# Kernel optimization log

Measured on AMD Instinct MI355X. Metric: run time of the kernel, lower is better.

The kernel has to match this reference:

```python
import jax, jax.numpy as jnp
import numpy as np

# db4 analysis filters (pywt convention); synthesis reuses same filters (orthogonal wavelet,
# correlation analysis + convolution synthesis gives perfect reconstruction under periodization).
DEC_LO = [-0.010597401784997278, 0.032883011666982945, 0.030841381835986965, -0.18703481171888114,
          -0.02798376941698385, 0.6308807679295904, 0.7148465705525415, 0.23037781330885523]
DEC_HI = [-0.23037781330885523, 0.7148465705525415, -0.6308807679295904, -0.02798376941698385,
          0.18703481171888114, 0.030841381835986965, -0.032883011666982945, -0.010597401784997278]
LEVELS = 3

def _analysis(x, filt):
    # a[n] = sum_k filt[k] * x[(2n+k) mod L]  (circular filter + downsample-by-2)
    y = sum(c * jnp.roll(x, -k, axis=-1) for k, c in enumerate(filt))
    return y[..., ::2]

def _synthesis(a, filt):
    # upsample-by-2 (zeros at odd positions) then circular convolution with filt
    u = jnp.zeros(a.shape[:-1] + (2 * a.shape[-1],), a.dtype).at[..., ::2].set(a)
    return sum(c * jnp.roll(u, k, axis=-1) for k, c in enumerate(filt))

def _decompose(z, levels):
    details, cur = [], z
    for _ in range(levels):
        details.append(_analysis(cur, DEC_HI))
        cur = _analysis(cur, DEC_LO)
    return cur, details

def _reconstruct(approx, details):
    cur = approx
    for d in reversed(details):
        cur = _synthesis(cur, DEC_LO) + _synthesis(d, DEC_HI)
    return cur

def _soft_threshold(c, lam_raw):
    # dynamic per-(batch,channel) threshold scaled by learnable softplus(lam_raw)
    lam = jax.nn.softplus(lam_raw) * jnp.mean(jnp.abs(c), axis=-1)  # [B,H]
    thr = jnp.sign(c) * jnp.maximum(jnp.abs(c) - lam[..., None], 0.0)
    return thr, lam

def _film(c, flow_raw, Wgb, bgb, Wg, bg):
    # FiLM gamma/beta from flow features, sigmoid-gated
    gb = flow_raw @ Wgb.T + bgb                      # [B, 2H]
    H = c.shape[1]
    gamma, beta = gb[:, :H], gb[:, H:]
    gate = jax.nn.sigmoid(flow_raw @ Wg + bg)[:, None, None]  # [B,1,1]
    return c * (1.0 + gate * gamma[:, :, None]) + gate * beta[:, :, None]

def setup_inputs() -> dict:
    key = jax.random.key(0)
    ks = jax.random.split(key, 8)
    B, L, C, Hd = 16, 4096, 64, 128
    x = jax.random.normal(ks[0], (B, L, C), jnp.float32)
    mask = jnp.ones((B, L), jnp.float32)
    flow_raw = jax.random.normal(ks[1], (B, 24), jnp.float32)
    W_in = jax.random.normal(ks[2], (Hd, C), jnp.float32) / np.sqrt(C)
    b_in = jnp.zeros((Hd,), jnp.float32)
    W_mix = jax.random.normal(ks[3], (Hd, Hd), jnp.float32) / np.sqrt(Hd)
    b_mix = jnp.zeros((Hd,), jnp.float32)
    lam_raw = jnp.full((LEVELS + 1,), 0.5413248538970947, jnp.float32)  # softplus^-1(1.0)
    film_Wgb = jax.random.normal(ks[4], (LEVELS + 1, 2 * Hd, 24), jnp.float32) * 0.05
    film_bgb = jnp.zeros((LEVELS + 1, 2 * Hd), jnp.float32)
    film_Wg = jax.random.normal(ks[5], (LEVELS + 1, 24), jnp.float32) * 0.05
    film_bg = jnp.zeros((LEVELS + 1,), jnp.float32)
    return dict(x=x, mask=mask, flow_raw=flow_raw, W_in=W_in, b_in=b_in, W_mix=W_mix, b_mix=b_mix,
                lam_raw=lam_raw, film_Wgb=film_Wgb, film_bgb=film_bgb, film_Wg=film_Wg, film_bg=film_bg)

def reference(x, mask, flow_raw, W_in, b_in, W_mix, b_mix, lam_raw, film_Wgb, film_bgb, film_Wg, film_bg):
    xp = x.transpose(0, 2, 1) * mask[:, None, :]               # [B,C,L]
    z = jnp.einsum('hc,bcl->bhl', W_in, xp) + b_in[:, None]    # input_proj (1x1 conv)
    approx, details = _decompose(z, LEVELS)
    approx = _film(approx, flow_raw, film_Wgb[0], film_bgb[0], film_Wg[0], film_bg[0])
    details = [_film(d, flow_raw, film_Wgb[i + 1], film_bgb[i + 1], film_Wg[i + 1], film_bg[i + 1])
               for i, d in enumerate(details)]
    approx_t, lam_a = _soft_threshold(approx, lam_raw[0])
    dts, lams = [], [lam_a]
    for i, d in enumerate(details):
        dt, lam_d = _soft_threshold(d, lam_raw[i + 1])
        dts.append(dt)
        lams.append(lam_d)
    z_rec = _reconstruct(approx_t, dts)
    mixed = jnp.einsum('gh,bhl->bgl', W_mix, z + z_rec) + b_mix[:, None]  # mix (1x1 conv)
    out = jax.nn.gelu(mixed, approximate=False)                 # torch nn.GELU is exact
    h_seq = out.transpose(0, 2, 1) * mask[..., None]            # [B,L,H]
    denom = jnp.clip(jnp.sum(mask, axis=1, keepdims=True), 1.0, None)
    h_pool = jnp.sum(h_seq * mask[..., None], axis=1) / denom   # masked mean pool [B,H]
    lam_cat = jnp.concatenate([l.reshape(l.shape[0], -1) for l in lams], axis=1)
    return h_seq, h_pool, jnp.mean(lam_cat, axis=1), jnp.max(lam_cat, axis=1)
```

## Files before the change

### kernel.cpp

```cpp
#include <hip/hip_runtime.h>
#include <math.h>

#define BB 16
#define LL 4096
#define CC 64
#define HD 128

typedef __attribute__((ext_vector_type(8))) short short8;
typedef __attribute__((ext_vector_type(8))) unsigned short ushort8;
typedef __attribute__((ext_vector_type(4))) float floatx4;

__constant__ float c_lo[8] = {
    -0.010597401784997278f, 0.032883011666982945f, 0.030841381835986965f,
    -0.18703481171888114f, -0.02798376941698385f, 0.6308807679295904f,
    0.7148465705525415f, 0.23037781330885523f};
__constant__ float c_hi[8] = {
    -0.23037781330885523f, 0.7148465705525415f, -0.6308807679295904f,
    -0.02798376941698385f, 0.18703481171888114f, 0.030841381835986965f,
    -0.032883011666982945f, -0.010597401784997278f};

__device__ __forceinline__ float gelu_exact(float x) {
    return 0.5f * x * (1.0f + erff(x * 0.70710678118654752440f));
}
__device__ __forceinline__ unsigned short f2b(float f) {
    unsigned int u = __float_as_uint(f);
    u = u + 0x7FFFu + ((u >> 16) & 1u);
    return (unsigned short)(u >> 16);
}
__device__ __forceinline__ float b2f(unsigned short s) {
    return __uint_as_float(((unsigned int)s) << 16);
}


__global__ __launch_bounds__(256) void prep_kernel(
    const float* __restrict__ W_in, unsigned short* __restrict__ Ain,
    const float* __restrict__ W_mix, unsigned short* __restrict__ Bmix,
    const float* __restrict__ flow, const float* __restrict__ Wgb,
    const float* __restrict__ bgb, const float* __restrict__ Wg,
    const float* __restrict__ bg, float* __restrict__ film_ws,
    float* __restrict__ gate_ws,
    const float* __restrict__ mask, float* __restrict__ denom) {
    __shared__ float red[256];
    int blk = blockIdx.x;
    int tid = threadIdx.x;
    if (blk < 32) {
        int q = blk * 256 + tid;
        int h = (q >> 3) & 127;
        int c = ((q >> 10) << 3) | (q & 7);
        Ain[q] = f2b(W_in[h * CC + c]);
    } else if (blk < 96) {
        int q = (blk - 32) * 256 + tid;
        int g = (q >> 3) & 127;
        int h = ((q >> 10) << 3) | (q & 7);
        Bmix[q] = f2b(W_mix[g * HD + h]);
    } else if (blk < 160) {
        int bf = blk - 96;
        int f = bf & 3;
        int b = bf >> 2;
        const float* fl = flow + b * 24;
        const float* wrow = Wgb + ((size_t)(f * 256 + tid)) * 24;
        float acc = bgb[f * 256 + tid];
#pragma unroll
        for (int j = 0; j < 24; ++j) acc = fmaf(wrow[j], fl[j], acc);
        film_ws[(size_t)bf * 256 + tid] = acc;
        if (tid == 0) {
            float g = bg[f];
#pragma unroll
            for (int j = 0; j < 24; ++j) g = fmaf(Wg[f * 24 + j], fl[j], g);
            gate_ws[bf] = 1.0f / (1.0f + expf(-g));
        }
    } else {
        int b = blk - 160;
        float s = 0.f;
        for (int i = tid; i < LL; i += 256) s += mask[(size_t)b * LL + i];
        red[tid] = s; __syncthreads();
        for (int st = 128; st > 0; st >>= 1) {
            if (tid < st) red[tid] += red[tid + st];
            __syncthreads();
        }
        if (tid == 0) denom[b] = fmaxf(red[0], 1.0f);
    }
}


__global__ __launch_bounds__(256) void zproj_kernel(const float* __restrict__ x,
                                                    const float* __restrict__ mask,
                                                    const unsigned short* __restrict__ Ain,
                                                    const float* __restrict__ b_in,
                                                    unsigned short* __restrict__ z_bf) {
    int blk = blockIdx.x;
    int b = blk >> 6;
    int l0 = (blk & 63) << 6;
    int tid = threadIdx.x;
    int lane = tid & 63;
    int w = tid >> 6;
    int h_half = w >> 1;
    int l_q = w & 1;
    int ln15 = lane & 15, lq4 = lane >> 4;

    int lr0 = l0 + l_q * 32 + ln15;
    int lr1 = lr0 + 16;
    float mk0 = mask[(size_t)b * LL + lr0];
    float mk1 = mask[(size_t)b * LL + lr1];

    floatx4 acc[4][2];
#pragma unroll
    for (int i = 0; i < 4; ++i)
#pragma unroll
        for (int j = 0; j < 2; ++j) acc[i][j] = (floatx4){0.f, 0.f, 0.f, 0.f};

#pragma unroll
    for (int ks = 0; ks < 2; ++ks) {
        int c0 = ks * 32 + (lq4 << 3);
        short8 bf0, bf1;
        {
            const float* xp = x + ((size_t)b * LL + lr0) * CC + c0;
            float4 xa = *(const float4*)xp;
            float4 xb = *(const float4*)(xp + 4);
            bf0[0] = (short)f2b(xa.x * mk0); bf0[1] = (short)f2b(xa.y * mk0);
            bf0[2] = (short)f2b(xa.z * mk0); bf0[3] = (short)f2b(xa.w * mk0);
            bf0[4] = (short)f2b(xb.x * mk0); bf0[5] = (short)f2b(xb.y * mk0);
            bf0[6] = (short)f2b(xb.z * mk0); bf0[7] = (short)f2b(xb.w * mk0);
        }
        {
            const float* xp = x + ((size_t)b * LL + lr1) * CC + c0;
            float4 xa = *(const float4*)xp;
            float4 xb = *(const float4*)(xp + 4);
            bf1[0] = (short)f2b(xa.x * mk1); bf1[1] = (short)f2b(xa.y * mk1);
            bf1[2] = (short)f2b(xa.z * mk1); bf1[3] = (short)f2b(xa.w * mk1);
            bf1[4] = (short)f2b(xb.x * mk1); bf1[5] = (short)f2b(xb.y * mk1);
            bf1[6] = (short)f2b(xb.z * mk1); bf1[7] = (short)f2b(xb.w * mk1);
        }
        int koct = ks * 4 + lq4;
#pragma unroll
        for (int ht = 0; ht < 4; ++ht) {
            short8 af = *(const short8*)(Ain + (size_t)koct * 1024 +
                                         (h_half * 64 + ht * 16 + ln15) * 8);
            acc[ht][0] = __builtin_amdgcn_mfma_f32_16x16x32_bf16(af, bf0, acc[ht][0], 0, 0, 0);
            acc[ht][1] = __builtin_amdgcn_mfma_f32_16x16x32_bf16(af, bf1, acc[ht][1], 0, 0, 0);
        }
    }

#pragma unroll
    for (int ht = 0; ht < 4; ++ht) {
#pragma unroll
        for (int r = 0; r < 4; ++r) {
            int h = h_half * 64 + ht * 16 + (lq4 << 2) + r;
            float bi = b_in[h];
            z_bf[((size_t)(b * HD + h)) * LL + lr0] = f2b(acc[ht][0][r] + bi);
            z_bf[((size_t)(b * HD + h)) * LL + lr1] = f2b(acc[ht][1][r] + bi);
        }
    }
}

__device__ __forceinline__ void analysis_step(const float* __restrict__ src,
                                              float* __restrict__ lo_dst,
                                              float* __restrict__ hi_dst,
                                              int half, int tid) {
    int len = half << 1;
    for (int q = tid; q < (half >> 2); q += 256) {
        int n0 = q << 2;
        float lo[4], hi[4];
        if (n0 + 4 == half) {
#pragma unroll
            for (int i = 0; i < 4; ++i) {
                float l = 0.f, hh = 0.f;
#pragma unroll
                for (int k = 0; k < 8; ++k) {
                    float v = src[(2 * (n0 + i) + k) & (len - 1)];
                    l = fmaf(c_lo[k], v, l);
                    hh = fmaf(c_hi[k], v, hh);
                }
                lo[i] = l; hi[i] = hh;
            }
        } else {
            float sv[16];
            const float* sp = src + (n0 << 1);
            *(float4*)&sv[0]  = *(const float4*)(sp);
            *(float4*)&sv[4]  = *(const float4*)(sp + 4);
            *(float4*)&sv[8]  = *(const float4*)(sp + 8);
            *(float4*)&sv[12] = *(const float4*)(sp + 12);
#pragma unroll
            for (int i = 0; i < 4; ++i) {
                float l = 0.f, hh = 0.f;
#pragma unroll
                for (int k = 0; k < 8; ++k) {
                    l = fmaf(c_lo[k], sv[2 * i + k], l);
                    hh = fmaf(c_hi[k], sv[2 * i + k], hh);
                }
                lo[i] = l; hi[i] = hh;
            }
        }
        *(float4*)&lo_dst[n0] = make_float4(lo[0], lo[1], lo[2], lo[3]);
        *(float4*)&hi_dst[n0] = make_float4(hi[0], hi[1], hi[2], hi[3]);
    }
}

__device__ __forceinline__ void synth_oct(const float* __restrict__ A,
                                          const float* __restrict__ D,
                                          int m0, int half, float* ov) {
    if (m0 == 0) {
        int mask2 = (half << 1) - 1;
#pragma unroll
        for (int t = 0; t < 8; ++t) {
            int par = t & 1;
            float s = 0.f;
#pragma unroll
            for (int j = 0; j < 4; ++j) {
                int k = 2 * j + par;
                int idx = ((t - k) & mask2) >> 1;
                s = fmaf(c_lo[k], A[idx], s);
                s = fmaf(c_hi[k], D[idx], s);
            }
            ov[t] = s;
        }
    } else {
        float av[8], dv[8];
        *(float4*)&av[0] = *(const float4*)(A + m0 - 4);
        *(float4*)&av[4] = *(const float4*)(A + m0);
        *(float4*)&dv[0] = *(const float4*)(D + m0 - 4);
        *(float4*)&dv[4] = *(const float4*)(D + m0);
#pragma unroll
        for (int t = 0; t < 4; ++t) {
            float e = 0.f, o = 0.f;
#pragma unroll
            for (int j = 0; j < 4; ++j) {
                float xa = av[t + 4 - j], xd = dv[t + 4 - j];
                e = fmaf(c_lo[2 * j], xa, e);     e = fmaf(c_hi[2 * j], xd, e);
                o = fmaf(c_lo[2 * j + 1], xa, o); o = fmaf(c_hi[2 * j + 1], xd, o);
            }
            ov[2 * t] = e;
            ov[2 * t + 1] = o;
        }
    }
}

__device__ __forceinline__ void synth_step(const float* __restrict__ A,
                                           const float* __restrict__ D,
                                           float* __restrict__ dst,
                                           int half, int tid) {
    for (int q = tid; q < (half >> 2); q += 256) {
        int m0 = q << 2;
        int i0 = m0 << 1;
        float ov[8];
        synth_oct(A, D, m0, half, ov);
        *(float4*)&dst[i0]     = make_float4(ov[0], ov[1], ov[2], ov[3]);
        *(float4*)&dst[i0 + 4] = make_float4(ov[4], ov[5], ov[6], ov[7]);
    }
}


__global__ __launch_bounds__(256) void wavelet_kernel(const unsigned short* __restrict__ z_bf,
                                                      unsigned short* __restrict__ s_bf,
                                                      const float* __restrict__ film_ws,
                                                      const float* __restrict__ gate_ws,
                                                      const float* __restrict__ lam_raw,
                                                      float* __restrict__ lam_ws) {
    __shared__ float zrow[4096];
    __shared__ float d1[2048];
    __shared__ float d2[1024];
    __shared__ float Aq[2048];
    __shared__ float Bq[1024];

    int blk = blockIdx.x;
    int b = blk >> 7;
    int h = blk & 127;
    int tid = threadIdx.x;
    const unsigned short* zg = z_bf + ((size_t)(b * HD + h)) * LL;
    unsigned short* sg = s_bf + ((size_t)(b * HD + h)) * LL;

    for (int i = tid; i < 512; i += 256) {
        ushort8 v = *(const ushort8*)(zg + (i << 3));
        *(float4*)&zrow[i << 3] =
            make_float4(b2f(v[0]), b2f(v[1]), b2f(v[2]), b2f(v[3]));
        *(float4*)&zrow[(i << 3) + 4] =
            make_float4(b2f(v[4]), b2f(v[5]), b2f(v[6]), b2f(v[7]));
    }
    __syncthreads();

    analysis_step(zrow, Aq, d1, 2048, tid);
    __syncthreads();
    analysis_step(Aq, Bq, d2, 1024, tid);
    __syncthreads();
    analysis_step(Bq, Aq, Aq + 512, 512, tid);
    __syncthreads();

    float sc0, sh0, sc1, sh1, sc2, sh2, sc3, sh3;
    {
        int base = b * 4;
#define FILM_COEF(bd, SC, SH)                                              \
        {   float ga = film_ws[((size_t)(base + bd)) * 256 + h];           \
            float be = film_ws[((size_t)(base + bd)) * 256 + 128 + h];     \
            float gt = gate_ws[base + bd];                                 \
            SC = 1.0f + gt * ga; SH = gt * be; }
        FILM_COEF(0, sc0, sh0) FILM_COEF(1, sc1, sh1)
        FILM_COEF(2, sc2, sh2) FILM_COEF(3, sc3, sh3)
#undef FILM_COEF
    }
    float s0 = 0.f, s1 = 0.f, s2 = 0.f, s3 = 0.f;
#define FILM4(P, LEN, SC, SH, SUM)                                         \
    for (int qq = tid; qq < ((LEN) >> 2); qq += 256) {                     \
        float4 v = *(float4*)&(P)[qq << 2];                                \
        v.x = fmaf(v.x, SC, SH); v.y = fmaf(v.y, SC, SH);                  \
        v.z = fmaf(v.z, SC, SH); v.w = fmaf(v.w, SC, SH);                  \
        *(float4*)&(P)[qq << 2] = v;                                       \
        SUM += fabsf(v.x) + fabsf(v.y) + fabsf(v.z) + fabsf(v.w);          \
    }
    FILM4(Aq, 512, sc0, sh0, s0)
    FILM4(d1, 2048, sc1, sh1, s1)
    FILM4(d2, 1024, sc2, sh2, s2)
    FILM4((Aq + 512), 512, sc3, sh3, s3)
#undef FILM4
#pragma unroll
    for (int off = 32; off > 0; off >>= 1) {
        s0 += __shfl_xor(s0, off);
        s1 += __shfl_xor(s1, off);
        s2 += __shfl_xor(s2, off);
        s3 += __shfl_xor(s3, off);
    }
    if ((tid & 63) == 0)
        ((float4*)Bq)[tid >> 6] = make_float4(s0, s1, s2, s3);
    __syncthreads();
    float4 r0 = ((const float4*)Bq)[0];
    float4 r1 = ((const float4*)Bq)[1];
    float4 r2 = ((const float4*)Bq)[2];
    float4 r3 = ((const float4*)Bq)[3];
    float lam0 = log1pf(expf(lam_raw[0])) * ((r0.x + r1.x + r2.x + r3.x) * (1.0f / 512.f));
    float lam1 = log1pf(expf(lam_raw[1])) * ((r0.y + r1.y + r2.y + r3.y) * (1.0f / 2048.f));
    float lam2 = log1pf(expf(lam_raw[2])) * ((r0.z + r1.z + r2.z + r3.z) * (1.0f / 1024.f));
    float lam3 = log1pf(expf(lam_raw[3])) * ((r0.w + r1.w + r2.w + r3.w) * (1.0f / 512.f));
    if (tid < 4) {
        float lam = (tid == 0) ? lam0 : (tid == 1) ? lam1 : (tid == 2) ? lam2 : lam3;
        lam_ws[((size_t)(b * 4 + tid)) * 128 + h] = lam;
    }
#define STHR4(P, LEN, LAM)                                                 \
    for (int qq = tid; qq < ((LEN) >> 2); qq += 256) {                     \
        float4 v = *(float4*)&(P)[qq << 2];                                \
        float a;                                                           \
        a = fabsf(v.x) - (LAM); v.x = (a > 0.f) ? copysignf(a, v.x) : 0.f; \
        a = fabsf(v.y) - (LAM); v.y = (a > 0.f) ? copysignf(a, v.y) : 0.f; \
        a = fabsf(v.z) - (LAM); v.z = (a > 0.f) ? copysignf(a, v.z) : 0.f; \
        a = fabsf(v.w) - (LAM); v.w = (a > 0.f) ? copysignf(a, v.w) : 0.f; \
        *(float4*)&(P)[qq << 2] = v;                                       \
    }
    STHR4(Aq, 512, lam0)
    STHR4(d1, 2048, lam1)
    STHR4(d2, 1024, lam2)
    STHR4((Aq + 512), 512, lam3)
#undef STHR4
    __syncthreads();

    synth_step(Aq, Aq + 512, Bq, 512, tid);
    __syncthreads();
    synth_step(Bq, d2, Aq, 1024, tid);
    __syncthreads();
    for (int q = tid; q < 512; q += 256) {
        int m0 = q << 2;
        int i0 = m0 << 1;
        float ov[8];
        synth_oct(Aq, d1, m0, 2048, ov);
        float zr[8];
        *(float4*)&zr[0] = *(float4*)&zrow[i0];
        *(float4*)&zr[4] = *(float4*)&zrow[i0 + 4];
        ushort8 o8;
#pragma unroll
        for (int t = 0; t < 8; ++t) o8[t] = f2b(ov[t] + zr[t]);
        *(ushort8*)(sg + i0) = o8;
    }
}


union U32x4S8 { unsigned int u[4]; short8 s; };

__global__ __launch_bounds__(256) void mix_kernel(const unsigned short* __restrict__ s_bf,
                                                  const unsigned short* __restrict__ Bmix,
                                                  const float* __restrict__ b_mix,
                                                  const float* __restrict__ mask,
                                                  float* __restrict__ out,
                                                  float* __restrict__ pool_part) {
    __shared__ unsigned int T[HD * 64];
    __shared__ float pbuf[2][HD];

    int blk = blockIdx.x;
    int b = blk >> 5;
    int lt128 = blk & 31;
    int l0 = lt128 << 7;
    int tid = threadIdx.x;
    int lane = tid & 63;
    int w = tid >> 6;
    int l_half = w >> 1, g_half = w & 1;
    int ln15 = lane & 15, lq4 = lane >> 4;

    {
        const unsigned int* src = (const unsigned int*)s_bf;
#pragma unroll
        for (int r = 0; r < 8; ++r) {
            int q = (r << 8) + tid;
            int hh = q >> 4;
            int k = q & 15;
            const unsigned int* gp = src + (size_t)(b * HD + hh) * (LL / 2) +
                                     (l0 >> 1) + (k << 2);
            uint4 v = *(const uint4*)gp;
            int sw = hh & 31;
            unsigned int* tp = T + hh * 64;
            tp[(4 * k + 0) ^ sw] = v.x;
            tp[(4 * k + 1) ^ sw] = v.y;
            tp[(4 * k + 2) ^ sw] = v.z;
            tp[(4 * k + 3) ^ sw] = v.w;
        }
    }
    __syncthreads();

    floatx4 acc[4][4];
#pragma unroll
    for (int i = 0; i < 4; ++i)
#pragma unroll
        for (int j = 0; j < 4; ++j) acc[i][j] = (floatx4){0.f, 0.f, 0.f, 0.f};

    const unsigned short* Bb = Bmix + (g_half * 64 + ln15) * 8;

#pragma unroll 2
    for (int ks = 0; ks < 4; ++ks) {
        int koct = ks * 4 + lq4;
        short8 a[4], bb[4];
#pragma unroll
        for (int lt = 0; lt < 4; ++lt) {
            int l_loc = l_half * 64 + lt * 16 + ln15;
            int lp = l_loc >> 1;
            int odd = l_loc & 1;
            U32x4S8 cv;
#pragma unroll
            for (int qq = 0; qq < 4; ++qq) {
                int h0 = koct * 8 + 2 * qq;
                unsigned int w0 = T[h0 * 64 + (lp ^ (h0 & 31))];
                unsigned int w1 = T[(h0 + 1) * 64 + (lp ^ ((h0 + 1) & 31))];
                unsigned int e0 = odd ? (w0 >> 16) : (w0 & 0xffffu);
                unsigned int e1 = odd ? (w1 >> 16) : (w1 & 0xffffu);
                cv.u[qq] = e0 | (e1 << 16);
            }
            a[lt] = cv.s;
        }
#pragma unroll
        for (int gt = 0; gt < 4; ++gt)
            bb[gt] = *(const short8*)(Bb + (size_t)koct * 1024 + gt * 128);
#pragma unroll
        for (int lt = 0; lt < 4; ++lt)
#pragma unroll
            for (int gt = 0; gt < 4; ++gt)
                acc[lt][gt] = __builtin_amdgcn_mfma_f32_16x16x32_bf16(a[lt], bb[gt], acc[lt][gt], 0, 0, 0);
    }

    int gcol[4]; float bmv[4]; float pacc[4];
#pragma unroll
    for (int gt = 0; gt < 4; ++gt) {
        gcol[gt] = g_half * 64 + gt * 16 + ln15;
        bmv[gt] = b_mix[gcol[gt]];
        pacc[gt] = 0.f;
    }
#pragma unroll
    for (int lt = 0; lt < 4; ++lt) {
#pragma unroll
        for (int r = 0; r < 4; ++r) {
            int l = l0 + l_half * 64 + lt * 16 + (lq4 << 2) + r;
            float mkv = mask[(size_t)b * LL + l];
            float* orow = out + ((size_t)b * LL + l) * HD;
#pragma unroll
            for (int gt = 0; gt < 4; ++gt) {
                float v = gelu_exact(acc[lt][gt][r] + bmv[gt]) * mkv;
                orow[gcol[gt]] = v;
                pacc[gt] = fmaf(v, mkv, pacc[gt]);
            }
        }
    }
#pragma unroll
    for (int gt = 0; gt < 4; ++gt) {
        pacc[gt] += __shfl_xor(pacc[gt], 16);
        pacc[gt] += __shfl_xor(pacc[gt], 32);
    }
    if (lane < 16) {
#pragma unroll
        for (int gt = 0; gt < 4; ++gt)
            pbuf[l_half][g_half * 64 + gt * 16 + lane] = pacc[gt];
    }
    __syncthreads();
    if (tid < HD)
        pool_part[((size_t)(b * 32 + lt128)) * HD + tid] = pbuf[0][tid] + pbuf[1][tid];
}


__global__ void finalize_kernel(const float* __restrict__ pool_part,
                                const float* __restrict__ denom,
                                const float* __restrict__ lam_ws,
                                float* __restrict__ d_out) {
    const size_t OUT1 = (size_t)BB * LL * HD;
    const size_t OUT2 = OUT1 + (size_t)BB * HD;
    const size_t OUT3 = OUT2 + BB;
    int b = blockIdx.x, tid = threadIdx.x;
    __shared__ float rsum[256], rmax[256];
    if (tid < 128) {
        float s = 0.f;
        for (int blk = 0; blk < 32; ++blk)
            s += pool_part[((size_t)(b * 32 + blk)) * HD + tid];
        d_out[OUT1 + (size_t)b * HD + tid] = s / denom[b];
    }
    float v0 = lam_ws[(size_t)b * 512 + tid];
    float v1 = lam_ws[(size_t)b * 512 + 256 + tid];
    rsum[tid] = v0 + v1;
    rmax[tid] = fmaxf(v0, v1);
    __syncthreads();
    for (int st = 128; st > 0; st >>= 1) {
        if (tid < st) {
            rsum[tid] += rsum[tid + st];
            rmax[tid] = fmaxf(rmax[tid], rmax[tid + st]);
        }
        __syncthreads();
    }
    if (tid == 0) {
        d_out[OUT2 + b] = rsum[0] / 512.0f;
        d_out[OUT3 + b] = rmax[0];
    }
}


extern "C" void kernel_launch(void* const* d_in, const int* in_sizes, int n_in,
                              void* d_out, int out_size, void* d_ws, size_t ws_size,
                              hipStream_t stream) {
    (void)in_sizes; (void)n_in; (void)out_size; (void)ws_size;
    const float* x      = (const float*)d_in[0];
    const float* mask   = (const float*)d_in[1];
    const float* flow   = (const float*)d_in[2];
    const float* W_in   = (const float*)d_in[3];
    const float* b_in   = (const float*)d_in[4];
    const float* W_mix  = (const float*)d_in[5];
    const float* b_mix  = (const float*)d_in[6];
    const float* lam_raw= (const float*)d_in[7];
    const float* Wgb    = (const float*)d_in[8];
    const float* bgb    = (const float*)d_in[9];
    const float* Wg     = (const float*)d_in[10];
    const float* bg     = (const float*)d_in[11];

    unsigned short* z_bf = (unsigned short*)d_ws;
    unsigned short* s_bf = z_bf + (size_t)BB * HD * LL;
    float* film_ws   = (float*)(s_bf + (size_t)BB * HD * LL);
    float* gate_ws   = film_ws + BB * 4 * 256;
    float* lam_ws    = gate_ws + 64;
    float* denom_ws  = lam_ws + BB * 4 * 128;
    float* pool_part = denom_ws + 16;
    unsigned short* Ain  = (unsigned short*)(pool_part + BB * 32 * HD);
    unsigned short* Bmix = Ain + HD * CC;

    float* out = (float*)d_out;

    hipLaunchKernelGGL(prep_kernel, dim3(176), dim3(256), 0, stream,
                       W_in, Ain, W_mix, Bmix, flow, Wgb, bgb, Wg, bg,
                       film_ws, gate_ws, mask, denom_ws);
    hipLaunchKernelGGL(zproj_kernel, dim3(BB * (LL / 64)), dim3(256), 0, stream,
                       x, mask, Ain, b_in, z_bf);
    hipLaunchKernelGGL(wavelet_kernel, dim3(BB * HD), dim3(256), 0, stream,
                       z_bf, s_bf, film_ws, gate_ws, lam_raw, lam_ws);
    hipLaunchKernelGGL(mix_kernel, dim3(BB * (LL / 128)), dim3(256), 0, stream,
                       s_bf, Bmix, b_mix, mask, out, pool_part);
    hipLaunchKernelGGL(finalize_kernel, dim3(BB), dim3(256), 0, stream,
                       pool_part, denom_ws, lam_ws, out);
}
```

Measured before the change: 75.00 us.

## Fold prep kernel into zproj, halve mix tile, move mask sum to finalize

Removes the separate prep kernel launch. The Bmix conversion and FiLM/gate computation now run in extra blocks appended to the zproj grid. zproj reads W_in directly from fp32 and converts it to bf16 per wave instead of using a pre-converted buffer, and the mask denominator is now computed inside finalize. The mix kernel tile drops from 128 to 64 positions, which doubles its block count and halves its LDS, so finalize must sum twice as many pool partials. The trade is one fewer launch and more mix parallelism, in exchange for redundant weight conversion in zproj and more partial-sum traffic.

```diff
diff --git a/kernel.cpp b/kernel.cpp
--- a/kernel.cpp
+++ b/kernel.cpp
@@ -32,66 +32,47 @@
 }
 
 
-__global__ __launch_bounds__(256) void prep_kernel(
-    const float* __restrict__ W_in, unsigned short* __restrict__ Ain,
+__global__ __launch_bounds__(256) void zproj_kernel(
+    const float* __restrict__ x, const float* __restrict__ mask,
+    const float* __restrict__ W_in, const float* __restrict__ b_in,
+    unsigned short* __restrict__ z_bf,
     const float* __restrict__ W_mix, unsigned short* __restrict__ Bmix,
     const float* __restrict__ flow, const float* __restrict__ Wgb,
     const float* __restrict__ bgb, const float* __restrict__ Wg,
     const float* __restrict__ bg, float* __restrict__ film_ws,
-    float* __restrict__ gate_ws,
-    const float* __restrict__ mask, float* __restrict__ denom) {
-    __shared__ float red[256];
+    float* __restrict__ gate_ws) {
     int blk = blockIdx.x;
     int tid = threadIdx.x;
-    if (blk < 32) {
-        int q = blk * 256 + tid;
-        int h = (q >> 3) & 127;
-        int c = ((q >> 10) << 3) | (q & 7);
-        Ain[q] = f2b(W_in[h * CC + c]);
-    } else if (blk < 96) {
-        int q = (blk - 32) * 256 + tid;
-        int g = (q >> 3) & 127;
-        int h = ((q >> 10) << 3) | (q & 7);
-        Bmix[q] = f2b(W_mix[g * HD + h]);
-    } else if (blk < 160) {
-        int bf = blk - 96;
-        int f = bf & 3;
-        int b = bf >> 2;
-        const float* fl = flow + b * 24;
-        const float* wrow = Wgb + ((size_t)(f * 256 + tid)) * 24;
-        float acc = bgb[f * 256 + tid];
-#pragma unroll
-        for (int j = 0; j < 24; ++j) acc = fmaf(wrow[j], fl[j], acc);
-        film_ws[(size_t)bf * 256 + tid] = acc;
-        if (tid == 0) {
-            float g = bg[f];
-#pragma unroll
-            for (int j = 0; j < 24; ++j) g = fmaf(Wg[f * 24 + j], fl[j], g);
-            gate_ws[bf] = 1.0f / (1.0f + expf(-g));
-        }
-    } else {
-        int b = blk - 160;
-        float s = 0.f;
-        for (int i = tid; i < LL; i += 256) s += mask[(size_t)b * LL + i];
-        red[tid] = s; __syncthreads();
-        for (int st = 128; st > 0; st >>= 1) {
-            if (tid < st) red[tid] += red[tid + st];
-            __syncthreads();
-        }
-        if (tid == 0) denom[b] = fmaxf(red[0], 1.0f);
-    }
-}
-
-
-__global__ __launch_bounds__(256) void zproj_kernel(const float* __restrict__ x,
-                                                    const float* __restrict__ mask,
-                                                    const unsigned short* __restrict__ Ain,
-                                                    const float* __restrict__ b_in,
-                                                    unsigned short* __restrict__ z_bf) {
-    int blk = blockIdx.x;
+
+    if (blk >= BB * 64) {
+        int e = blk - BB * 64;
+        if (e < 64) {
+            int q = e * 256 + tid;
+            int g = (q >> 3) & 127;
+            int h = ((q >> 10) << 3) | (q & 7);
+            Bmix[q] = f2b(W_mix[g * HD + h]);
+        } else {
+            int bf = e - 64;
+            int f = bf & 3;
+            int b = bf >> 2;
+            const float* fl = flow + b * 24;
+            const float* wrow = Wgb + ((size_t)(f * 256 + tid)) * 24;
+            float acc = bgb[f * 256 + tid];
+#pragma unroll
+            for (int j = 0; j < 24; ++j) acc = fmaf(wrow[j], fl[j], acc);
+            film_ws[(size_t)bf * 256 + tid] = acc;
+            if (tid == 0) {
+                float g = bg[f];
+#pragma unroll
+                for (int j = 0; j < 24; ++j) g = fmaf(Wg[f * 24 + j], fl[j], g);
+                gate_ws[bf] = 1.0f / (1.0f + expf(-g));
+            }
+        }
+        return;
+    }
+
     int b = blk >> 6;
     int l0 = (blk & 63) << 6;
-    int tid = threadIdx.x;
     int lane = tid & 63;
     int w = tid >> 6;
     int h_half = w >> 1;
@@ -131,11 +112,18 @@
             bf1[4] = (short)f2b(xb.x * mk1); bf1[5] = (short)f2b(xb.y * mk1);
             bf1[6] = (short)f2b(xb.z * mk1); bf1[7] = (short)f2b(xb.w * mk1);
         }
-        int koct = ks * 4 + lq4;
+        int c8 = ks * 32 + (lq4 << 3);
+        const float* wb = W_in + (size_t)(h_half * 64 + ln15) * CC + c8;
 #pragma unroll
         for (int ht = 0; ht < 4; ++ht) {
-            short8 af = *(const short8*)(Ain + (size_t)koct * 1024 +
-                                         (h_half * 64 + ht * 16 + ln15) * 8);
+            const float* wr = wb + (size_t)ht * 16 * CC;
+            float4 wa = *(const float4*)wr;
+            float4 wc = *(const float4*)(wr + 4);
+            short8 af;
+            af[0] = (short)f2b(wa.x); af[1] = (short)f2b(wa.y);
+            af[2] = (short)f2b(wa.z); af[3] = (short)f2b(wa.w);
+            af[4] = (short)f2b(wc.x); af[5] = (short)f2b(wc.y);
+            af[6] = (short)f2b(wc.z); af[7] = (short)f2b(wc.w);
             acc[ht][0] = __builtin_amdgcn_mfma_f32_16x16x32_bf16(af, bf0, acc[ht][0], 0, 0, 0);
             acc[ht][1] = __builtin_amdgcn_mfma_f32_16x16x32_bf16(af, bf1, acc[ht][1], 0, 0, 0);
         }
@@ -152,6 +140,7 @@
         }
     }
 }
+
 
 __device__ __forceinline__ void analysis_step(const float* __restrict__ src,
                                               float* __restrict__ lo_dst,
@@ -378,13 +367,13 @@
                                                   const float* __restrict__ mask,
                                                   float* __restrict__ out,
                                                   float* __restrict__ pool_part) {
-    __shared__ unsigned int T[HD * 64];
+    __shared__ unsigned int T[HD * 32];
     __shared__ float pbuf[2][HD];
 
     int blk = blockIdx.x;
-    int b = blk >> 5;
-    int lt128 = blk & 31;
-    int l0 = lt128 << 7;
+    int b = blk >> 6;
+    int lt64 = blk & 63;
+    int l0 = lt64 << 6;
     int tid = threadIdx.x;
     int lane = tid & 63;
     int w = tid >> 6;
@@ -394,26 +383,25 @@
     {
         const unsigned int* src = (const unsigned int*)s_bf;
 #pragma unroll
-        for (int r = 0; r < 8; ++r) {
+        for (int r = 0; r < 4; ++r) {
             int q = (r << 8) + tid;
-            int hh = q >> 4;
-            int k = q & 15;
-            const unsigned int* gp = src + (size_t)(b * HD + hh) * (LL / 2) +
-                                     (l0 >> 1) + (k << 2);
-            uint4 v = *(const uint4*)gp;
+            int hh = q >> 3;
+            int k = q & 7;
+            uint4 v = *(const uint4*)(src + (size_t)(b * HD + hh) * (LL / 2) +
+                                      (l0 >> 1) + (k << 2));
             int sw = hh & 31;
-            unsigned int* tp = T + hh * 64;
-            tp[(4 * k + 0) ^ sw] = v.x;
-            tp[(4 * k + 1) ^ sw] = v.y;
-            tp[(4 * k + 2) ^ sw] = v.z;
-            tp[(4 * k + 3) ^ sw] = v.w;
-        }
-    }
-    __syncthreads();
-
-    floatx4 acc[4][4];
-#pragma unroll
-    for (int i = 0; i < 4; ++i)
+            unsigned int* tp = T + hh * 32;
+            tp[((k << 2) + 0) ^ sw] = v.x;
+            tp[((k << 2) + 1) ^ sw] = v.y;
+            tp[((k << 2) + 2) ^ sw] = v.z;
+            tp[((k << 2) + 3) ^ sw] = v.w;
+        }
+    }
+    __syncthreads();
+
+    floatx4 acc[2][4];
+#pragma unroll
+    for (int i = 0; i < 2; ++i)
 #pragma unroll
         for (int j = 0; j < 4; ++j) acc[i][j] = (floatx4){0.f, 0.f, 0.f, 0.f};
 
@@ -422,18 +410,18 @@
 #pragma unroll 2
     for (int ks = 0; ks < 4; ++ks) {
         int koct = ks * 4 + lq4;
-        short8 a[4], bb[4];
-#pragma unroll
-        for (int lt = 0; lt < 4; ++lt) {
-            int l_loc = l_half * 64 + lt * 16 + ln15;
+        short8 a[2], bb[4];
+#pragma unroll
+        for (int lt = 0; lt < 2; ++lt) {
+            int l_loc = l_half * 32 + lt * 16 + ln15;
             int lp = l_loc >> 1;
             int odd = l_loc & 1;
             U32x4S8 cv;
 #pragma unroll
             for (int qq = 0; qq < 4; ++qq) {
                 int h0 = koct * 8 + 2 * qq;
-                unsigned int w0 = T[h0 * 64 + (lp ^ (h0 & 31))];
-                unsigned int w1 = T[(h0 + 1) * 64 + (lp ^ ((h0 + 1) & 31))];
+                unsigned int w0 = T[h0 * 32 + (lp ^ (h0 & 31))];
+                unsigned int w1 = T[(h0 + 1) * 32 + (lp ^ ((h0 + 1) & 31))];
                 unsigned int e0 = odd ? (w0 >> 16) : (w0 & 0xffffu);
                 unsigned int e1 = odd ? (w1 >> 16) : (w1 & 0xffffu);
                 cv.u[qq] = e0 | (e1 << 16);
@@ -444,7 +432,7 @@
         for (int gt = 0; gt < 4; ++gt)
             bb[gt] = *(const short8*)(Bb + (size_t)koct * 1024 + gt * 128);
 #pragma unroll
-        for (int lt = 0; lt < 4; ++lt)
+        for (int lt = 0; lt < 2; ++lt)
 #pragma unroll
             for (int gt = 0; gt < 4; ++gt)
                 acc[lt][gt] = __builtin_amdgcn_mfma_f32_16x16x32_bf16(a[lt], bb[gt], acc[lt][gt], 0, 0, 0);
@@ -458,10 +446,10 @@
         pacc[gt] = 0.f;
     }
 #pragma unroll
-    for (int lt = 0; lt < 4; ++lt) {
+    for (int lt = 0; lt < 2; ++lt) {
 #pragma unroll
         for (int r = 0; r < 4; ++r) {
-            int l = l0 + l_half * 64 + lt * 16 + (lq4 << 2) + r;
+            int l = l0 + l_half * 32 + lt * 16 + (lq4 << 2) + r;
             float mkv = mask[(size_t)b * LL + l];
             float* orow = out + ((size_t)b * LL + l) * HD;
 #pragma unroll
@@ -484,12 +472,12 @@
     }
     __syncthreads();
     if (tid < HD)
-        pool_part[((size_t)(b * 32 + lt128)) * HD + tid] = pbuf[0][tid] + pbuf[1][tid];
+        pool_part[((size_t)(b * 64 + lt64)) * HD + tid] = pbuf[0][tid] + pbuf[1][tid];
 }
 
 
 __global__ void finalize_kernel(const float* __restrict__ pool_part,
-                                const float* __restrict__ denom,
+                                const float* __restrict__ mask,
                                 const float* __restrict__ lam_ws,
                                 float* __restrict__ d_out) {
     const size_t OUT1 = (size_t)BB * LL * HD;
@@ -497,12 +485,30 @@
     const size_t OUT3 = OUT2 + BB;
     int b = blockIdx.x, tid = threadIdx.x;
     __shared__ float rsum[256], rmax[256];
+    __shared__ float dsh;
+
+    float ms = 0.f;
+    const float4* mp = (const float4*)(mask + (size_t)b * LL);
+    for (int i = tid; i < LL / 4; i += 256) {
+        float4 m = mp[i];
+        ms += m.x + m.y + m.z + m.w;
+    }
+    rsum[tid] = ms; __syncthreads();
+    for (int st = 128; st > 0; st >>= 1) {
+        if (tid < st) rsum[tid] += rsum[tid + st];
+        __syncthreads();
+    }
+    if (tid == 0) dsh = fmaxf(rsum[0], 1.0f);
+    __syncthreads();
+    float denom = dsh;
+
     if (tid < 128) {
         float s = 0.f;
-        for (int blk = 0; blk < 32; ++blk)
-            s += pool_part[((size_t)(b * 32 + blk)) * HD + tid];
-        d_out[OUT1 + (size_t)b * HD + tid] = s / denom[b];
-    }
+        for (int blk = 0; blk < 64; ++blk)
+            s += pool_part[((size_t)(b * 64 + blk)) * HD + tid];
+        d_out[OUT1 + (size_t)b * HD + tid] = s / denom;
+    }
+
     float v0 = lam_ws[(size_t)b * 512 + tid];
     float v1 = lam_ws[(size_t)b * 512 + 256 + tid];
     rsum[tid] = v0 + v1;
@@ -544,22 +550,18 @@
     float* film_ws   = (float*)(s_bf + (size_t)BB * HD * LL);
     float* gate_ws   = film_ws + BB * 4 * 256;
     float* lam_ws    = gate_ws + 64;
-    float* denom_ws  = lam_ws + BB * 4 * 128;
-    float* pool_part = denom_ws + 16;
-    unsigned short* Ain  = (unsigned short*)(pool_part + BB * 32 * HD);
-    unsigned short* Bmix = Ain + HD * CC;
+    float* pool_part = lam_ws + BB * 4 * 128;
+    unsigned short* Bmix = (unsigned short*)(pool_part + BB * 64 * HD);
 
     float* out = (float*)d_out;
 
-    hipLaunchKernelGGL(prep_kernel, dim3(176), dim3(256), 0, stream,
-                       W_in, Ain, W_mix, Bmix, flow, Wgb, bgb, Wg, bg,
-                       film_ws, gate_ws, mask, denom_ws);
-    hipLaunchKernelGGL(zproj_kernel, dim3(BB * (LL / 64)), dim3(256), 0, stream,
-                       x, mask, Ain, b_in, z_bf);
+    hipLaunchKernelGGL(zproj_kernel, dim3(BB * 64 + 128), dim3(256), 0, stream,
+                       x, mask, W_in, b_in, z_bf,
+                       W_mix, Bmix, flow, Wgb, bgb, Wg, bg, film_ws, gate_ws);
     hipLaunchKernelGGL(wavelet_kernel, dim3(BB * HD), dim3(256), 0, stream,
                        z_bf, s_bf, film_ws, gate_ws, lam_raw, lam_ws);
-    hipLaunchKernelGGL(mix_kernel, dim3(BB * (LL / 128)), dim3(256), 0, stream,
+    hipLaunchKernelGGL(mix_kernel, dim3(BB * (LL / 64)), dim3(256), 0, stream,
                        s_bf, Bmix, b_mix, mask, out, pool_part);
     hipLaunchKernelGGL(finalize_kernel, dim3(BB), dim3(256), 0, stream,
-                       pool_part, denom_ws, lam_ws, out);
-}
+                       pool_part, mask, lam_ws, out);
+}
```

After: 74.17 us. Within noise of the previous version (-1.1%).
